# Kernel tuning notes

Measured on AMD Instinct MI355X. Metric: run time of the kernel, lower is better.

Reference implementation:

```python
import jax, jax.numpy as jnp
import numpy as np

# Hyperparameters from __init__ defaults / chosen init kwargs
GAMMA_NEG = 4.0
GAMMA_POS = 1.0
CLIP = 0.05
EPS = 1e-8
ALPHA1 = 2.0
ALPHA_OTHER = 0.5
TOP_K = 10

B, C = 2048, 9605


def setup_inputs() -> dict:
    key = jax.random.key(0)
    k_x, k_y, k_c, k_r, k_d, k_o = jax.random.split(key, 6)
    x = jax.random.normal(k_x, (B, C), dtype=jnp.float32)
    y = (jax.random.uniform(k_y, (B, C)) < 0.01).astype(jnp.float32)
    compost_idx = jax.random.randint(k_c, (30,), 0, C, dtype=jnp.int32)
    recycle_idx = jax.random.randint(k_r, (70,), 0, C, dtype=jnp.int32)
    donate_idx = jax.random.randint(k_d, (70,), 0, C, dtype=jnp.int32)
    other_idx = jax.random.randint(k_o, (40,), 0, C, dtype=jnp.int32)
    # dense whitelist mapping: 0 = not in W_human mapping; priority compost>recycle>donate
    wl_map = jnp.zeros((C,), dtype=jnp.int32)
    wl_map = wl_map.at[other_idx].set(4)
    wl_map = wl_map.at[donate_idx].set(3)
    wl_map = wl_map.at[recycle_idx].set(2)
    wl_map = wl_map.at[compost_idx].set(1)
    return {"x": x, "y": y, "compost_idx": compost_idx,
            "recycle_idx": recycle_idx, "donate_idx": donate_idx,
            "wl_map": wl_map}


def reference(x, y, compost_idx, recycle_idx, donate_idx, wl_map):
    b, c = x.shape
    xs_pos = jax.nn.sigmoid(x)
    xs_neg = jnp.minimum(1.0 - xs_pos + CLIP, 1.0)  # clip shift, clamp max=1
    # base asymmetric BCE term: y*log(p) + (1-y)*log(1-p+clip)
    base = (y * jnp.log(jnp.maximum(xs_pos, EPS))
            + (1.0 - y) * jnp.log(jnp.maximum(xs_neg, EPS)))  # [B, C]

    # per-sample ground-truth whitelist groups (find_gt_whitelist)
    has1 = jnp.sum(y[:, compost_idx], axis=1) > 0  # [B]
    has2 = jnp.sum(y[:, recycle_idx], axis=1) > 0
    has3 = jnp.sum(y[:, donate_idx], axis=1) > 0
    gt_only4 = ~(has1 | has2 | has3)  # gt_whitelist == [4]

    # top-10 predicted classes (argsort descending, first 10)
    _, top_idx = jax.lax.top_k(xs_pos, TOP_K)  # [B, 10]
    rows = jnp.arange(b)

    def step(carry, j):
        # j: [B] class index at current rank; sequential over rank (order matters)
        mult, found = carry
        wl = wl_map[j]                      # group id of this class, 0 if unmapped
        in_map = wl > 0
        in_gt = (((wl == 1) & has1) | ((wl == 2) & has2)
                 | ((wl == 3) & has3) | ((wl == 4) & gt_only4))
        f = jnp.where(in_map & gt_only4, ALPHA_OTHER, 1.0)
        f = f * jnp.where(in_map & (~in_gt) & (~found), ALPHA1, 1.0)
        mult = mult.at[rows, j].multiply(f)
        found = found | (in_map & in_gt)
        return (mult, found), None

    init = (jnp.ones((b, c), x.dtype), jnp.zeros((b,), dtype=bool))
    (mult, found), _ = jax.lax.scan(step, init, top_idx.T)  # scan over 10 ranks

    # if no gt-whitelist match found in top-10: multiply all top-10 by alpha1 again
    extra = jnp.where(found[:, None], 1.0, ALPHA1)  # [B, 1]
    mult = mult.at[rows[:, None], top_idx].multiply(
        jnp.broadcast_to(extra, (b, TOP_K)))

    # asymmetric focal weighting (computed without grad in original)
    pt = xs_pos * y + xs_neg * (1.0 - y)
    gamma = GAMMA_POS * y + GAMMA_NEG * (1.0 - y)
    w = jax.lax.stop_gradient(jnp.power(1.0 - pt, gamma))

    return -jnp.sum(base * mult * w)
```

## Files before the change

kernel.cpp:

```cpp
#include <hip/hip_runtime.h>

#define TOPK 10
#define CLIP 0.05f
#define EPSV 1e-8f
#define ALPHA1 2.0f
#define ALPHA_OTHER 0.5f
#define TCAND 2.5f
#define MAXC 512
#define LN2F 0.69314718056f

__device__ __forceinline__ unsigned long long pack_vc(float v, int c, int C) {
  unsigned u = __float_as_uint(v);
  unsigned key = (u & 0x80000000u) ? ~u : (u | 0x80000000u);
  return ((unsigned long long)key << 32) | (unsigned)(C - c);
}
__device__ __forceinline__ float unpack_v(unsigned long long p) {
  unsigned key = (unsigned)(p >> 32);
  unsigned u = (key & 0x80000000u) ? (key & 0x7fffffffu) : ~key;
  return __uint_as_float(u);
}
__device__ __forceinline__ int unpack_c(unsigned long long p, int C) {
  return C - (int)(unsigned)(p & 0xffffffffu);
}

__device__ __forceinline__ float base_w(float xv, bool pos) {
  float u = __expf(-xv);
  float r = __builtin_amdgcn_rcpf(1.f + u);
  float xneg = fminf(1.05f - r, 1.f);
  float q = pos ? r : xneg;
  float b2 = __log2f(fmaxf(q, EPSV));
  float t = 1.f - q;
  float t2 = t * t;
  float w = pos ? t : t2 * t2;
  return b2 * w;
}

__device__ __forceinline__ void proc4(float4 X, float4 Y, float4& acc,
                                      unsigned& cmask, int slot) {
  acc.x += base_w(X.x, Y.x > 0.5f);
  acc.y += base_w(X.y, Y.y > 0.5f);
  acc.z += base_w(X.z, Y.z > 0.5f);
  acc.w += base_w(X.w, Y.w > 0.5f);
  float mx = fmaxf(fmaxf(X.x, X.y), fmaxf(X.z, X.w));
  cmask |= (mx > TCAND ? 1u : 0u) << slot;
}

__global__ __launch_bounds__(256) void asl_kernel(
    const float* __restrict__ x, const float* __restrict__ y,
    const int* __restrict__ compost, const int* __restrict__ recycle,
    const int* __restrict__ donate, const int* __restrict__ wl_map,
    float* __restrict__ out, int C, int n1, int n2, int n3)
{
  const int row = blockIdx.x;
  const float* xr = x + (size_t)row * (size_t)C;
  const float* yr = y + (size_t)row * (size_t)C;
  const int tid = threadIdx.x;
  const int lane = tid & 63;
  const int wave = tid >> 6;

  __shared__ int s_has[3];
  __shared__ unsigned s_cnt;
  __shared__ unsigned long long s_cand[MAXC];
  __shared__ float s_sum[4];
  __shared__ unsigned long long s_top[TOPK];

  if (tid < 3) s_has[tid] = 0;
  if (tid == 0) s_cnt = 0;
  __syncthreads();

  const int ntot = n1 + n2 + n3;
  float gflag = 0.f; int gwhich = -1;
  if (tid < ntot) {
    int colI;
    if (tid < n1)           { gwhich = 0; colI = compost[tid]; }
    else if (tid < n1 + n2) { gwhich = 1; colI = recycle[tid - n1]; }
    else                    { gwhich = 2; colI = donate[tid - n1 - n2]; }
    gflag = yr[colI];
  }

  float ssc = 0.f;

#define PUSH(V, CCOL)                                                     \
  do {                                                                    \
    unsigned _i = atomicAdd(&s_cnt, 1u);                                  \
    if (_i < MAXC) s_cand[_i] = pack_vc((V), (CCOL), C);                  \
  } while (0)
#define PROC_DIRECT(XV, YV, COL)                                          \
  do {                                                                    \
    float _xv = (XV);                                                     \
    ssc += base_w(_xv, (YV) > 0.5f);                                      \
    if (_xv > TCAND) PUSH(_xv, (COL));                                    \
  } while (0)

  int lead = (int)((4u - ((unsigned)((size_t)row * (size_t)C) & 3u)) & 3u);
  if (lead > C) lead = C;
  for (int col = tid; col < lead; col += 256) PROC_DIRECT(xr[col], yr[col], col);

  const int nvec = (C - lead) >> 2;
  const float4* __restrict__ x4 = (const float4*)(xr + lead);
  const float4* __restrict__ y4 = (const float4*)(yr + lead);

  float4 sacc = make_float4(0.f, 0.f, 0.f, 0.f);
  unsigned cmask = 0;

  int slotbase = 0;
  for (int base = tid; base < nvec; base += 1024, slotbase += 4) {
    const bool v1 = base + 256 < nvec;
    const bool v2 = base + 512 < nvec;
    const bool v3 = base + 768 < nvec;
    float4 xv0, xv1, xv2, xv3, yv0, yv1, yv2, yv3;
    xv0 = x4[base];                 yv0 = y4[base];
    if (v1) { xv1 = x4[base + 256]; yv1 = y4[base + 256]; }
    if (v2) { xv2 = x4[base + 512]; yv2 = y4[base + 512]; }
    if (v3) { xv3 = x4[base + 768]; yv3 = y4[base + 768]; }
    proc4(xv0, yv0, sacc, cmask, slotbase + 0);
    if (v1) proc4(xv1, yv1, sacc, cmask, slotbase + 1);
    if (v2) proc4(xv2, yv2, sacc, cmask, slotbase + 2);
    if (v3) proc4(xv3, yv3, sacc, cmask, slotbase + 3);
  }

  for (int col = lead + nvec * 4 + tid; col < C; col += 256)
    PROC_DIRECT(xr[col], yr[col], col);

  if (gwhich >= 0 && gflag > 0.5f) s_has[gwhich] = 1;
  for (int i = 256 + tid; i < ntot; i += 256) {
    int which, colI;
    if (i < n1)           { which = 0; colI = compost[i]; }
    else if (i < n1 + n2) { which = 1; colI = recycle[i - n1]; }
    else                  { which = 2; colI = donate[i - n1 - n2]; }
    if (yr[colI] > 0.5f) s_has[which] = 1;
  }

  while (cmask) {
    int b = __ffs(cmask) - 1;
    cmask &= cmask - 1;
    int o = b >> 2, j = b & 3;
    int i = tid + o * 1024 + j * 256;
    float4 X = x4[i];
    int cb = lead + i * 4;
    if (X.x > TCAND) PUSH(X.x, cb + 0);
    if (X.y > TCAND) PUSH(X.y, cb + 1);
    if (X.z > TCAND) PUSH(X.z, cb + 2);
    if (X.w > TCAND) PUSH(X.w, cb + 3);
  }
#undef PROC_DIRECT
#undef PUSH

  float sum = ssc + sacc.x + sacc.y + sacc.z + sacc.w;
#pragma unroll
  for (int off = 32; off > 0; off >>= 1) sum += __shfl_xor(sum, off, 64);
  if (lane == 0) s_sum[wave] = sum;
  __syncthreads();

  if (wave == 0) {
    const unsigned cnt = s_cnt;
    unsigned long long ls[TOPK];
#pragma unroll
    for (int s = 0; s < TOPK; s++) ls[s] = 0ULL;

#define INSERT(P)                                                          \
    do {                                                                   \
      unsigned long long _p = (P);                                         \
      if (_p > ls[TOPK - 1]) {                                             \
        _Pragma("unroll")                                                  \
        for (int _s = 0; _s < TOPK; _s++) {                                \
          bool _g = _p > ls[_s];                                           \
          unsigned long long _t = _g ? ls[_s] : _p;                        \
          ls[_s] = _g ? _p : ls[_s];                                       \
          _p = _t;                                                         \
        }                                                                  \
      }                                                                    \
    } while (0)

    if (cnt >= TOPK && cnt <= MAXC) {
      for (unsigned i = lane; i < cnt; i += 64) INSERT(s_cand[i]);
    } else {
      for (int col = lane; col < C; col += 64) INSERT(pack_vc(xr[col], col, C));
    }
#undef INSERT

    for (int r = 0; r < TOPK; r++) {
      unsigned long long mine = ls[0];
      unsigned long long best = mine;
#pragma unroll
      for (int off = 32; off > 0; off >>= 1) {
        unsigned long long o = __shfl_xor(best, off, 64);
        best = (o > best) ? o : best;
      }
      if (lane == 0) s_top[r] = best;
      if (mine == best) {
#pragma unroll
        for (int s = 0; s < TOPK - 1; s++) ls[s] = ls[s + 1];
        ls[TOPK - 1] = 0ULL;
      }
    }
  }
  __syncthreads();

  if (tid == 0) {
    float total = s_sum[0] + s_sum[1] + s_sum[2] + s_sum[3];
    const bool h1 = s_has[0] != 0, h2 = s_has[1] != 0, h3 = s_has[2] != 0;
    const bool gt4 = !(h1 || h2 || h3);

    bool found = false;
    float fr[TOPK];
#pragma unroll
    for (int r = 0; r < TOPK; r++) {
      int col = unpack_c(s_top[r], C);
      int wl = wl_map[col];
      bool in_map = wl > 0;
      bool in_gt = (wl == 1 && h1) || (wl == 2 && h2) ||
                   (wl == 3 && h3) || (wl == 4 && gt4);
      float f = 1.f;
      if (in_map && gt4) f *= ALPHA_OTHER;
      if (in_map && !in_gt && !found) f *= ALPHA1;
      fr[r] = f;
      found = found || (in_map && in_gt);
    }
    const float extra = found ? 1.f : ALPHA1;
#pragma unroll
    for (int r = 0; r < TOPK; r++) {
      float mult = fr[r] * extra;
      if (mult != 1.f) {
        int col = unpack_c(s_top[r], C);
        float xv = unpack_v(s_top[r]);
        float bwv = base_w(xv, yr[col] > 0.5f);
        total += (mult - 1.f) * bwv;
      }
    }
    atomicAdd(out, -total * LN2F);
  }
}

extern "C" void kernel_launch(void* const* d_in, const int* in_sizes, int n_in,
                              void* d_out, int out_size, void* d_ws, size_t ws_size,
                              hipStream_t stream) {
  const float* x       = (const float*)d_in[0];
  const float* y       = (const float*)d_in[1];
  const int*   compost = (const int*)d_in[2];
  const int*   recycle = (const int*)d_in[3];
  const int*   donate  = (const int*)d_in[4];
  const int*   wl_map  = (const int*)d_in[5];
  float* out = (float*)d_out;

  const int C  = in_sizes[5];
  const int B  = in_sizes[0] / C;
  const int n1 = in_sizes[2], n2 = in_sizes[3], n3 = in_sizes[4];

  hipMemsetAsync(out, 0, sizeof(float), stream);
  asl_kernel<<<B, 256, 0, stream>>>(x, y, compost, recycle, donate, wl_map,
                                    out, C, n1, n2, n3);
}
```

Before: 206.8 us.

## Stream x/y tiles through double-buffered LDS via direct global-to-LDS loads

Replaces the register-based float4 streaming loop with a double-buffered pipeline that uses global_load_lds to copy 1024-float tiles of x and y straight into shared memory, overlapping the next tile's load with compute on the current one. Threads then read scalars from LDS and push candidates inline, which removes the candidate bitmask and the second global pass. The candidate buffer is halved to 256 entries. The cost is extra LDS traffic and explicit vmcnt waits, and there is a risk the smaller candidate buffer overflows. Each wave consumes only the LDS region its own loads filled, so no block barrier is used between tiles.

```diff
diff --git a/kernel.cpp b/kernel.cpp
--- a/kernel.cpp
+++ b/kernel.cpp
@@ -6,7 +6,7 @@
 #define ALPHA1 2.0f
 #define ALPHA_OTHER 0.5f
 #define TCAND 2.5f
-#define MAXC 512
+#define MAXC 256
 #define LN2F 0.69314718056f
 
 __device__ __forceinline__ unsigned long long pack_vc(float v, int c, int C) {
@@ -35,15 +35,6 @@
   return b2 * w;
 }
 
-__device__ __forceinline__ void proc4(float4 X, float4 Y, float4& acc,
-                                      unsigned& cmask, int slot) {
-  acc.x += base_w(X.x, Y.x > 0.5f);
-  acc.y += base_w(X.y, Y.y > 0.5f);
-  acc.z += base_w(X.z, Y.z > 0.5f);
-  acc.w += base_w(X.w, Y.w > 0.5f);
-  float mx = fmaxf(fmaxf(X.x, X.y), fmaxf(X.z, X.w));
-  cmask |= (mx > TCAND ? 1u : 0u) << slot;
-}
 
 __global__ __launch_bounds__(256) void asl_kernel(
     const float* __restrict__ x, const float* __restrict__ y,
@@ -58,6 +49,8 @@
   const int lane = tid & 63;
   const int wave = tid >> 6;
 
+  __shared__ float s_x[2][1024];
+  __shared__ float s_y[2][1024];
   __shared__ int s_has[3];
   __shared__ unsigned s_cnt;
   __shared__ unsigned long long s_cand[MAXC];
@@ -96,30 +89,58 @@
   if (lead > C) lead = C;
   for (int col = tid; col < lead; col += 256) PROC_DIRECT(xr[col], yr[col], col);
 
-  const int nvec = (C - lead) >> 2;
+  const int nvec  = (C - lead) >> 2;
+  const int nvec4 = nvec << 2;
   const float4* __restrict__ x4 = (const float4*)(xr + lead);
   const float4* __restrict__ y4 = (const float4*)(yr + lead);
-
-  float4 sacc = make_float4(0.f, 0.f, 0.f, 0.f);
-  unsigned cmask = 0;
-
-  int slotbase = 0;
-  for (int base = tid; base < nvec; base += 1024, slotbase += 4) {
-    const bool v1 = base + 256 < nvec;
-    const bool v2 = base + 512 < nvec;
-    const bool v3 = base + 768 < nvec;
-    float4 xv0, xv1, xv2, xv3, yv0, yv1, yv2, yv3;
-    xv0 = x4[base];                 yv0 = y4[base];
-    if (v1) { xv1 = x4[base + 256]; yv1 = y4[base + 256]; }
-    if (v2) { xv2 = x4[base + 512]; yv2 = y4[base + 512]; }
-    if (v3) { xv3 = x4[base + 768]; yv3 = y4[base + 768]; }
-    proc4(xv0, yv0, sacc, cmask, slotbase + 0);
-    if (v1) proc4(xv1, yv1, sacc, cmask, slotbase + 1);
-    if (v2) proc4(xv2, yv2, sacc, cmask, slotbase + 2);
-    if (v3) proc4(xv3, yv3, sacc, cmask, slotbase + 3);
-  }
-
-  for (int col = lead + nvec * 4 + tid; col < C; col += 256)
+  const int ntiles = (nvec + 255) >> 8;
+
+  const unsigned wl4 = (unsigned)(wave * 64 + lane);
+  const int wbase = wave * 256;
+
+#define STAGE(T, B)                                                          \
+  do {                                                                       \
+    unsigned _g4 = (unsigned)(T) * 256u + wl4;                               \
+    if (_g4 >= (unsigned)nvec) _g4 = (unsigned)nvec - 1u;     \
+    __builtin_amdgcn_global_load_lds(                                        \
+        (__attribute__((address_space(1))) void*)(void*)(x4 + _g4),          \
+        (__attribute__((address_space(3))) void*)(&s_x[(B)][wbase]),         \
+        16, 0, 0);                                                           \
+    __builtin_amdgcn_global_load_lds(                                        \
+        (__attribute__((address_space(1))) void*)(void*)(y4 + _g4),          \
+        (__attribute__((address_space(3))) void*)(&s_y[(B)][wbase]),         \
+        16, 0, 0);                                                           \
+  } while (0)
+
+  float acc[4] = {0.f, 0.f, 0.f, 0.f};
+
+  if (ntiles > 0) {
+    STAGE(0, 0);
+    int buf = 0;
+    for (int t = 0; t < ntiles; ++t) {
+      if (t + 1 < ntiles) {
+        STAGE(t + 1, buf ^ 1);
+        asm volatile("s_waitcnt vmcnt(2)" ::: "memory");
+      } else {
+        asm volatile("s_waitcnt vmcnt(0)" ::: "memory");
+      }
+      const int tb = t * 1024 + wbase;
+#pragma unroll
+      for (int k = 0; k < 4; ++k) {
+        const int off  = k * 64 + lane;
+        const int fidx = tb + off;
+        if (fidx < nvec4) {
+          float xv = s_x[buf][wbase + off];
+          float yv = s_y[buf][wbase + off];
+          acc[k] += base_w(xv, yv > 0.5f);
+          if (xv > TCAND) PUSH(xv, lead + fidx);
+        }
+      }
+      buf ^= 1;
+    }
+  }
+
+  for (int col = lead + nvec4 + tid; col < C; col += 256)
     PROC_DIRECT(xr[col], yr[col], col);
 
   if (gwhich >= 0 && gflag > 0.5f) s_has[gwhich] = 1;
@@ -130,23 +151,11 @@
     else                  { which = 2; colI = donate[i - n1 - n2]; }
     if (yr[colI] > 0.5f) s_has[which] = 1;
   }
-
-  while (cmask) {
-    int b = __ffs(cmask) - 1;
-    cmask &= cmask - 1;
-    int o = b >> 2, j = b & 3;
-    int i = tid + o * 1024 + j * 256;
-    float4 X = x4[i];
-    int cb = lead + i * 4;
-    if (X.x > TCAND) PUSH(X.x, cb + 0);
-    if (X.y > TCAND) PUSH(X.y, cb + 1);
-    if (X.z > TCAND) PUSH(X.z, cb + 2);
-    if (X.w > TCAND) PUSH(X.w, cb + 3);
-  }
 #undef PROC_DIRECT
 #undef PUSH
-
-  float sum = ssc + sacc.x + sacc.y + sacc.z + sacc.w;
+#undef STAGE
+
+  float sum = ssc + acc[0] + acc[1] + acc[2] + acc[3];
 #pragma unroll
   for (int off = 32; off > 0; off >>= 1) sum += __shfl_xor(sum, off, 64);
   if (lane == 0) s_sum[wave] = sum;
```

Result: slower. 211.4 us (+2.2%).
